# Optimization experiments

Hardware: AMD Instinct MI355X
Metric: run time of the kernel (lower is better)

## Reference

```python
import jax, jax.numpy as jnp
import numpy as np

B, C, H, W = 16, 64, 128, 128
K = 3  # dynamic kernel size


def setup_inputs() -> dict:
    key = jax.random.key(0)
    ks = jax.random.split(key, 6)
    return {
        "x": jax.random.normal(ks[0], (B, C, H, W), jnp.float32),       # feature map
        "d": jax.random.normal(ks[1], (B, 64), jnp.float32),            # degradation repr
        "Wk1": jax.random.normal(ks[2], (64, 64), jnp.float32) * 0.05,  # Linear(64,64), no bias
        "Wk2": jax.random.normal(ks[3], (64 * K * K, 64), jnp.float32) * 0.05,  # Linear(64,576)
        "Wc": jax.random.normal(ks[4], (64, 64), jnp.float32) * 0.05,   # 1x1 conv weight (out,in)
        "bc": jnp.zeros((64,), jnp.float32),                            # 1x1 conv bias
    }


def _lrelu(v):
    return jnp.where(v >= 0, v, 0.1 * v)


def reference(x, d, Wk1, Wk2, Wc, bc):
    b, c, h, w = x.shape
    k = K
    # kernel-generating MLP: Linear -> LeakyReLU(0.1) -> Linear
    hid = _lrelu(d @ Wk1.T)                      # (B, 64)
    kern = (hid @ Wk2.T).reshape(b, c, 1, k, k)   # one 3x3 kernel per (batch, channel)

    # dynamic depthwise 3x3 conv: per-sample kernels, groups == channels
    def dwconv(xi, ki):
        # xi: (C,H,W), ki: (C,1,3,3) in OIHW with feature_group_count=C
        return jax.lax.conv_general_dilated(
            xi[None], ki, window_strides=(1, 1), padding='SAME',
            feature_group_count=c,
            dimension_numbers=('NCHW', 'OIHW', 'NCHW'))[0]

    out = jax.vmap(dwconv)(x, kern)              # (B,C,H,W)
    out = _lrelu(out)
    # 1x1 pointwise conv with bias
    out = jnp.einsum('bchw,oc->bohw', out, Wc) + bc[None, :, None, None]
    return out
```

## Files before the change

### kernel.cpp

```cpp
#include <hip/hip_runtime.h>

#define Bn 16
#define Cn 64
#define Hn 128
#define Wn 128
#define HWn (Hn * Wn)

typedef __attribute__((ext_vector_type(8)))  short  short8;
typedef __attribute__((ext_vector_type(16))) float  floatx16;
typedef __attribute__((ext_vector_type(4)))  float  floatx4;
using int32x4 = int __attribute__((ext_vector_type(4)));

__device__ float
llvm_amdgcn_raw_buffer_load_fp32(int32x4 srsrc, int voffset, int soffset,
                                 int aux) __asm("llvm.amdgcn.raw.buffer.load.f32");
__device__ floatx4
llvm_amdgcn_raw_buffer_load_v4f32(int32x4 srsrc, int voffset, int soffset,
                                  int aux) __asm("llvm.amdgcn.raw.buffer.load.v4f32");

__device__ __forceinline__ int32x4 make_rsrc(const void* p, int bytes) {
    int32x4 r;
    r.x = (int)(unsigned)(uintptr_t)p;
    r.y = (int)((uintptr_t)p >> 32);
    r.z = bytes;
    r.w = 0x00020000;
    return r;
}

__device__ __forceinline__ unsigned short f2bf(float f) {
    unsigned u = __float_as_uint(f);
    u += 0x7fffu + ((u >> 16) & 1u);
    return (unsigned short)(u >> 16);
}
__device__ __forceinline__ float lrelu(float v) { return v >= 0.f ? v : 0.1f * v; }

__global__ __launch_bounds__(192)
void gen_kern6(const float* __restrict__ d,
               const float* __restrict__ Wk1,
               const float* __restrict__ Wk2,
               const float* __restrict__ Wc,
               float* __restrict__ kernP,
               unsigned short* __restrict__ WcBF) {
    const int b = blockIdx.x;
    const int r = blockIdx.y;
    const int t = threadIdx.x;
    __shared__ float hid_s[64];

    if (t < 64) {
        const float4* __restrict__ w4 = (const float4*)(Wk1 + (size_t)t * 64);
        const float*  __restrict__ db = d + b * 64;
        float s0 = 0.f, s1 = 0.f, s2 = 0.f, s3 = 0.f;
        #pragma unroll
        for (int j = 0; j < 16; ++j) {
            const float4 wv = w4[j];
            s0 += db[4 * j + 0] * wv.x;
            s1 += db[4 * j + 1] * wv.y;
            s2 += db[4 * j + 2] * wv.z;
            s3 += db[4 * j + 3] * wv.w;
        }
        hid_s[t] = lrelu((s0 + s1) + (s2 + s3));
    }
    __syncthreads();

    {
        const int o = r * 192 + t;
        const float4* __restrict__ w4 = (const float4*)(Wk2 + (size_t)o * 64);
        const float4* __restrict__ h4 = (const float4*)hid_s;
        float s0 = 0.f, s1 = 0.f, s2 = 0.f, s3 = 0.f;
        #pragma unroll
        for (int j = 0; j < 16; ++j) {
            const float4 wv = w4[j];
            const float4 hv = h4[j];
            s0 += hv.x * wv.x;
            s1 += hv.y * wv.y;
            s2 += hv.z * wv.z;
            s3 += hv.w * wv.w;
        }
        const int c = o / 9, tap = o - c * 9;
        kernP[b * 768 + c * 12 + tap] = (s0 + s1) + (s2 + s3);
    }

    if (b == 0 && r == 0) {
        for (int idx = t; idx < 4096; idx += 192)
            WcBF[idx] = f2bf(Wc[idx]);
    }
}

__global__ __launch_bounds__(256)
void da_mfma2(const float* __restrict__ x,
              const float* __restrict__ kernP,
              const unsigned short* __restrict__ WcBF,
              const float* __restrict__ bc,
              float* __restrict__ out) {
    const int t    = threadIdx.x;
    const int lane = t & 63;
    const int wv   = t >> 6;
    const int col  = lane & 31;
    const int kh   = lane >> 5;
    const int bx   = blockIdx.x;
    const int h    = ((bx & 7) << 4) | (bx >> 3);
    const int b    = blockIdx.y;

    __shared__ float tl[16 * 3 * 136];

    int rofsB[3];
    #pragma unroll
    for (int i = 0; i < 3; ++i) {
        const int hh = h + i - 1;
        rofsB[i] = (hh >= 0 && hh < Hn) ? hh * (Wn * 4) : 0x10000000;
    }

    const int32x4 rs = make_rsrc(x + (size_t)b * Cn * HWn, Cn * HWn * 4);

    floatx16 acc[2];
    #pragma unroll
    for (int m = 0; m < 2; ++m)
        #pragma unroll
        for (int r = 0; r < 16; ++r)
            acc[m][r] = bc[m * 32 + (r & 3) + 8 * (r >> 2) + 4 * kh];

    const int sch = t >> 4;
    const int px0 = (t & 15) * 8;
    const float* __restrict__ kp = kernP + b * 768;

    const int px = wv * 32 + col;

    for (int g = 0; g < 4; ++g) {
        const int c = g * 16 + sch;
        const floatx4* k4 = (const floatx4*)(kp + c * 12);
        const floatx4 k0 = k4[0];
        const floatx4 k1 = k4[1];
        const float   k8 = ((const float*)k4)[8];

        float xa[3][8];
        #pragma unroll
        for (int r = 0; r < 3; ++r) {
            const int vo = (c << 16) + rofsB[r] + px0 * 4;
            const floatx4 va = llvm_amdgcn_raw_buffer_load_v4f32(rs, vo, 0, 0);
            const floatx4 vb = llvm_amdgcn_raw_buffer_load_v4f32(rs, vo + 16, 0, 0);
            xa[r][0] = va.x; xa[r][1] = va.y; xa[r][2] = va.z; xa[r][3] = va.w;
            xa[r][4] = vb.x; xa[r][5] = vb.y; xa[r][6] = vb.z; xa[r][7] = vb.w;
        }

        float t0[8], t1[8], t2[8];
        #pragma unroll
        for (int i = 0; i < 8; ++i) {
            t0[i] = k0.x * xa[0][i] + k0.w * xa[1][i] + k1.z * xa[2][i];
            t1[i] = k0.y * xa[0][i] + k1.x * xa[1][i] + k1.w * xa[2][i];
            t2[i] = k0.z * xa[0][i] + k1.y * xa[1][i] + k8   * xa[2][i];
        }
        {
            const int base = (sch * 3) * 136 + 4 + px0;
            *(float4*)&tl[base]             = make_float4(t0[0], t0[1], t0[2], t0[3]);
            *(float4*)&tl[base + 4]         = make_float4(t0[4], t0[5], t0[6], t0[7]);
            *(float4*)&tl[base + 136]       = make_float4(t1[0], t1[1], t1[2], t1[3]);
            *(float4*)&tl[base + 140]       = make_float4(t1[4], t1[5], t1[6], t1[7]);
            *(float4*)&tl[base + 272]       = make_float4(t2[0], t2[1], t2[2], t2[3]);
            *(float4*)&tl[base + 276]       = make_float4(t2[4], t2[5], t2[6], t2[7]);
        }
        if (t < 96) {
            const int ch = t / 6, rem = t - ch * 6;
            const int dx = rem >> 1, side = rem & 1;
            tl[(ch * 3 + dx) * 136 + (side ? 132 : 3)] = 0.f;
        }
        __syncthreads();

        short8 bfr;
        #pragma unroll
        for (int j = 0; j < 8; ++j) {
            const int cl = kh * 8 + j;
            const int base = (cl * 3) * 136 + 4 + px;
            const float dw = tl[base - 1]
                           + tl[base + 136]
                           + tl[base + 273];
            bfr[j] = (short)f2bf(lrelu(dw));
        }
        const short8 a0 = *(const short8*)(WcBF + (0 * 32 + col) * 64 + g * 16 + kh * 8);
        const short8 a1 = *(const short8*)(WcBF + (1 * 32 + col) * 64 + g * 16 + kh * 8);
        acc[0] = __builtin_amdgcn_mfma_f32_32x32x16_bf16(a0, bfr, acc[0], 0, 0, 0);
        acc[1] = __builtin_amdgcn_mfma_f32_32x32x16_bf16(a1, bfr, acc[1], 0, 0, 0);
        __syncthreads();
    }

    float* __restrict__ ob = out + (size_t)b * Cn * HWn + h * Wn + px;
    #pragma unroll
    for (int m = 0; m < 2; ++m)
        #pragma unroll
        for (int r = 0; r < 16; ++r) {
            const int o = m * 32 + (r & 3) + 8 * (r >> 2) + 4 * kh;
            ob[(size_t)o * HWn] = acc[m][r];
        }
}

extern "C" void kernel_launch(void* const* d_in, const int* in_sizes, int n_in,
                              void* d_out, int out_size, void* d_ws, size_t ws_size,
                              hipStream_t stream) {
    const float* x   = (const float*)d_in[0];
    const float* d   = (const float*)d_in[1];
    const float* Wk1 = (const float*)d_in[2];
    const float* Wk2 = (const float*)d_in[3];
    const float* Wc  = (const float*)d_in[4];
    const float* bc  = (const float*)d_in[5];
    float* out = (float*)d_out;
    float*          kernP = (float*)d_ws;
    unsigned short* WcBF  = (unsigned short*)((float*)d_ws + Bn * 768);

    gen_kern6<<<dim3(Bn, 3), dim3(192), 0, stream>>>(d, Wk1, Wk2, Wc, kernP, WcBF);
    da_mfma2<<<dim3(Hn, Bn), dim3(256), 0, stream>>>(x, kernP, WcBF, bc, out);
}
```

Baseline: 138.2 us.

## Double-buffer depthwise LDS tile and prefetch next channel group's input

The LDS tile is double-buffered, so each channel group's stencil partials go to alternating buffers and one of the two barriers per iteration is removed. The next group's x rows and dynamic kernel taps are loaded right after the barrier, overlapping global loads with the LDS reduction and MFMA. Wc bf16 fragments for all groups are hoisted into registers up front, halo zeros are written once, and launch bounds request 3 blocks per CU. The cost is more registers and twice the LDS per block, which may limit occupancy.

```diff
diff --git a/kernel.cpp b/kernel.cpp
--- a/kernel.cpp
+++ b/kernel.cpp
@@ -11,9 +11,6 @@
 typedef __attribute__((ext_vector_type(4)))  float  floatx4;
 using int32x4 = int __attribute__((ext_vector_type(4)));
 
-__device__ float
-llvm_amdgcn_raw_buffer_load_fp32(int32x4 srsrc, int voffset, int soffset,
-                                 int aux) __asm("llvm.amdgcn.raw.buffer.load.f32");
 __device__ floatx4
 llvm_amdgcn_raw_buffer_load_v4f32(int32x4 srsrc, int voffset, int soffset,
                                   int aux) __asm("llvm.amdgcn.raw.buffer.load.v4f32");
@@ -86,8 +83,8 @@
     }
 }
 
-__global__ __launch_bounds__(256)
-void da_mfma2(const float* __restrict__ x,
+__global__ __launch_bounds__(256, 3)
+void da_mfma3(const float* __restrict__ x,
               const float* __restrict__ kernP,
               const unsigned short* __restrict__ WcBF,
               const float* __restrict__ bc,
@@ -101,7 +98,7 @@
     const int h    = ((bx & 7) << 4) | (bx >> 3);
     const int b    = blockIdx.y;
 
-    __shared__ float tl[16 * 3 * 136];
+    __shared__ float tl[2][16 * 3 * 136];
 
     int rofsB[3];
     #pragma unroll
@@ -112,6 +109,21 @@
 
     const int32x4 rs = make_rsrc(x + (size_t)b * Cn * HWn, Cn * HWn * 4);
 
+    if (t < 192) {
+        const int bi = t >= 96 ? 1 : 0;
+        const int r  = t - bi * 96;
+        const int ch = r / 6, rem = r - ch * 6;
+        const int dx = rem >> 1, side = rem & 1;
+        tl[bi][(ch * 3 + dx) * 136 + (side ? 132 : 3)] = 0.f;
+    }
+
+    short8 afr[2][4];
+    #pragma unroll
+    for (int m = 0; m < 2; ++m)
+        #pragma unroll
+        for (int g = 0; g < 4; ++g)
+            afr[m][g] = *(const short8*)(WcBF + (m * 32 + col) * 64 + g * 16 + kh * 8);
+
     floatx16 acc[2];
     #pragma unroll
     for (int m = 0; m < 2; ++m)
@@ -122,17 +134,12 @@
     const int sch = t >> 4;
     const int px0 = (t & 15) * 8;
     const float* __restrict__ kp = kernP + b * 768;
-
     const int px = wv * 32 + col;
 
-    for (int g = 0; g < 4; ++g) {
-        const int c = g * 16 + sch;
-        const floatx4* k4 = (const floatx4*)(kp + c * 12);
-        const floatx4 k0 = k4[0];
-        const floatx4 k1 = k4[1];
-        const float   k8 = ((const float*)k4)[8];
-
-        float xa[3][8];
+    float xa[3][8];
+    floatx4 kc0, kc1; float kc8;
+    {
+        const int c = sch;
         #pragma unroll
         for (int r = 0; r < 3; ++r) {
             const int vo = (c << 16) + rofsB[r] + px0 * 4;
@@ -141,45 +148,58 @@
             xa[r][0] = va.x; xa[r][1] = va.y; xa[r][2] = va.z; xa[r][3] = va.w;
             xa[r][4] = vb.x; xa[r][5] = vb.y; xa[r][6] = vb.z; xa[r][7] = vb.w;
         }
+        const floatx4* k4 = (const floatx4*)(kp + c * 12);
+        kc0 = k4[0]; kc1 = k4[1]; kc8 = ((const float*)k4)[8];
+    }
+
+    #pragma unroll
+    for (int g = 0; g < 4; ++g) {
+        float* __restrict__ tb = tl[g & 1];
 
         float t0[8], t1[8], t2[8];
         #pragma unroll
         for (int i = 0; i < 8; ++i) {
-            t0[i] = k0.x * xa[0][i] + k0.w * xa[1][i] + k1.z * xa[2][i];
-            t1[i] = k0.y * xa[0][i] + k1.x * xa[1][i] + k1.w * xa[2][i];
-            t2[i] = k0.z * xa[0][i] + k1.y * xa[1][i] + k8   * xa[2][i];
+            t0[i] = kc0.x * xa[0][i] + kc0.w * xa[1][i] + kc1.z * xa[2][i];
+            t1[i] = kc0.y * xa[0][i] + kc1.x * xa[1][i] + kc1.w * xa[2][i];
+            t2[i] = kc0.z * xa[0][i] + kc1.y * xa[1][i] + kc8   * xa[2][i];
         }
         {
             const int base = (sch * 3) * 136 + 4 + px0;
-            *(float4*)&tl[base]             = make_float4(t0[0], t0[1], t0[2], t0[3]);
-            *(float4*)&tl[base + 4]         = make_float4(t0[4], t0[5], t0[6], t0[7]);
-            *(float4*)&tl[base + 136]       = make_float4(t1[0], t1[1], t1[2], t1[3]);
-            *(float4*)&tl[base + 140]       = make_float4(t1[4], t1[5], t1[6], t1[7]);
-            *(float4*)&tl[base + 272]       = make_float4(t2[0], t2[1], t2[2], t2[3]);
-            *(float4*)&tl[base + 276]       = make_float4(t2[4], t2[5], t2[6], t2[7]);
-        }
-        if (t < 96) {
-            const int ch = t / 6, rem = t - ch * 6;
-            const int dx = rem >> 1, side = rem & 1;
-            tl[(ch * 3 + dx) * 136 + (side ? 132 : 3)] = 0.f;
+            *(float4*)&tb[base]       = make_float4(t0[0], t0[1], t0[2], t0[3]);
+            *(float4*)&tb[base + 4]   = make_float4(t0[4], t0[5], t0[6], t0[7]);
+            *(float4*)&tb[base + 136] = make_float4(t1[0], t1[1], t1[2], t1[3]);
+            *(float4*)&tb[base + 140] = make_float4(t1[4], t1[5], t1[6], t1[7]);
+            *(float4*)&tb[base + 272] = make_float4(t2[0], t2[1], t2[2], t2[3]);
+            *(float4*)&tb[base + 276] = make_float4(t2[4], t2[5], t2[6], t2[7]);
         }
         __syncthreads();
+
+        if (g < 3) {
+            const int c = (g + 1) * 16 + sch;
+            #pragma unroll
+            for (int r = 0; r < 3; ++r) {
+                const int vo = (c << 16) + rofsB[r] + px0 * 4;
+                const floatx4 va = llvm_amdgcn_raw_buffer_load_v4f32(rs, vo, 0, 0);
+                const floatx4 vb = llvm_amdgcn_raw_buffer_load_v4f32(rs, vo + 16, 0, 0);
+                xa[r][0] = va.x; xa[r][1] = va.y; xa[r][2] = va.z; xa[r][3] = va.w;
+                xa[r][4] = vb.x; xa[r][5] = vb.y; xa[r][6] = vb.z; xa[r][7] = vb.w;
+            }
+            const floatx4* k4 = (const floatx4*)(kp + c * 12);
+            kc0 = k4[0]; kc1 = k4[1]; kc8 = ((const float*)k4)[8];
+        }
 
         short8 bfr;
         #pragma unroll
         for (int j = 0; j < 8; ++j) {
             const int cl = kh * 8 + j;
-            const int base = (cl * 3) * 136 + 4 + px;
-            const float dw = tl[base - 1]
-                           + tl[base + 136]
-                           + tl[base + 273];
+            const int bse = (cl * 3) * 136 + 4 + px;
+            const float dw = tb[bse - 1]
+                           + tb[bse + 136]
+                           + tb[bse + 273];
             bfr[j] = (short)f2bf(lrelu(dw));
         }
-        const short8 a0 = *(const short8*)(WcBF + (0 * 32 + col) * 64 + g * 16 + kh * 8);
-        const short8 a1 = *(const short8*)(WcBF + (1 * 32 + col) * 64 + g * 16 + kh * 8);
-        acc[0] = __builtin_amdgcn_mfma_f32_32x32x16_bf16(a0, bfr, acc[0], 0, 0, 0);
-        acc[1] = __builtin_amdgcn_mfma_f32_32x32x16_bf16(a1, bfr, acc[1], 0, 0, 0);
-        __syncthreads();
+        acc[0] = __builtin_amdgcn_mfma_f32_32x32x16_bf16(afr[0][g], bfr, acc[0], 0, 0, 0);
+        acc[1] = __builtin_amdgcn_mfma_f32_32x32x16_bf16(afr[1][g], bfr, acc[1], 0, 0, 0);
     }
 
     float* __restrict__ ob = out + (size_t)b * Cn * HWn + h * Wn + px;
@@ -206,5 +226,5 @@
     unsigned short* WcBF  = (unsigned short*)((float*)d_ws + Bn * 768);
 
     gen_kern6<<<dim3(Bn, 3), dim3(192), 0, stream>>>(d, Wk1, Wk2, Wc, kernP, WcBF);
-    da_mfma2<<<dim3(Hn, Bn), dim3(256), 0, stream>>>(x, kernP, WcBF, bc, out);
-}
+    da_mfma3<<<dim3(Hn, Bn), dim3(256), 0, stream>>>(x, kernP, WcBF, bc, out);
+}
```

Result: no change. 138.7 us (+0.4%).
